# Performance work log

Measured on AMD Instinct MI355X. Metric: run time of the kernel, lower is better.

## Reference

```python
import jax, jax.numpy as jnp
import numpy as np

N_ENTS = 50000
N_EDGES = 500000
N_RELS = 200
RANK = 128
N_LAYERS = 2
RRELU_SLOPE = (1.0 / 8.0 + 1.0 / 3.0) / 2.0  # F.rrelu eval-mode: mean of default lower/upper


def setup_inputs() -> dict:
    key = jax.random.key(0)
    ks = jax.random.split(key, 9)
    return {
        "ent_emb": jax.random.normal(ks[0], (N_ENTS, RANK), dtype=jnp.float32),
        "rel_emb": jax.random.normal(ks[1], (N_RELS, RANK), dtype=jnp.float32),
        "norm": jax.random.uniform(ks[2], (N_ENTS, 1), dtype=jnp.float32),
        "Wn": jax.random.normal(ks[3], (N_LAYERS, RANK, RANK), dtype=jnp.float32) * 0.05,
        "Wl": jax.random.normal(ks[4], (N_LAYERS, RANK, RANK), dtype=jnp.float32) * 0.05,
        "Wa": jax.random.normal(ks[5], (N_LAYERS, RANK, RANK), dtype=jnp.float32) * 0.05,
        "src": jax.random.randint(ks[6], (N_EDGES,), 0, N_ENTS, dtype=jnp.int32),
        "dst": jax.random.randint(ks[7], (N_EDGES,), 0, N_ENTS, dtype=jnp.int32),
        "etype": jax.random.randint(ks[8], (N_EDGES,), 0, N_RELS, dtype=jnp.int32),
    }


def reference(ent_emb, rel_emb, norm, Wn, Wl, Wa, src, dst, etype):
    n = ent_emb.shape[0]
    # in-degree mask (same graph across layers)
    in_deg = jax.ops.segment_sum(jnp.ones_like(dst, dtype=jnp.float32), dst, num_segments=n)
    has_in = (in_deg > 0)[:, None]  # [N,1]
    h = ent_emb
    for l in range(Wn.shape[0]):
        # edge gather + add + linear: msg = (h[src] + rel_emb[etype]) @ Wn[l]
        msg = (h[src] + rel_emb[etype]) @ Wn[l]  # [E, rank]
        # scatter-sum into destination nodes, then per-node norm
        agg = jax.ops.segment_sum(msg, dst, num_segments=n) * norm  # [N, rank]
        # masked self-loop: loop_weight where in_degree>0, else alone_loop_weight
        loop = jnp.where(has_in, h @ Wl[l], h @ Wa[l])
        h = agg + loop
        # rrelu in eval mode == leaky relu with slope (1/8 + 1/3)/2
        h = jnp.where(h >= 0, h, h * RRELU_SLOPE)
        # dropout=0.0 -> identity
    return h
```

## Files before the change

### kernel.cpp

```cpp
#include <hip/hip_runtime.h>

#define SLOPE 0.22916666666666666f
#define ALONE_CAP 2048

typedef __attribute__((ext_vector_type(8))) short bfrag;
typedef __attribute__((ext_vector_type(4))) float ffrag;

__device__ __forceinline__ unsigned short rne16(float f) {
    unsigned u = __float_as_uint(f);
    return (unsigned short)((u + 0x7FFFu + ((u >> 16) & 1u)) >> 16);
}
__device__ __forceinline__ float bf2f(unsigned short h) {
    return __uint_as_float(((unsigned)h) << 16);
}
__device__ __forceinline__ unsigned packsplit(float f) {
    unsigned short hi = rne16(f);
    unsigned short lo = rne16(f - bf2f(hi));
    return ((unsigned)hi << 16) | lo;
}
__device__ __forceinline__ float recon(unsigned u) {
    return __uint_as_float(u & 0xFFFF0000u) + __uint_as_float(u << 16);
}
__device__ __forceinline__ float4 recon4(uint4 u) {
    return make_float4(recon(u.x), recon(u.y), recon(u.z), recon(u.w));
}

__global__ __launch_bounds__(256) void prep_kernel(
    const int* __restrict__ dst, int* __restrict__ deg, int e, int eb,
    const float* __restrict__ ent, unsigned* __restrict__ Esp,
    int total4, int cb,
    const float* __restrict__ Wn, const float* __restrict__ Wl,
    ushort* __restrict__ packW) {
    int b = blockIdx.x;
    if (b < eb) {
        int i = b * 256 + threadIdx.x;
        if (i < e) atomicAdd(&deg[dst[i]], 1);
    } else if (b < eb + cb) {
        int i = (b - eb) * 256 + threadIdx.x;
        if (i >= total4) return;
        float4 v = ((const float4*)ent)[i];
        uint4 w;
        w.x = packsplit(v.x); w.y = packsplit(v.y);
        w.z = packsplit(v.z); w.w = packsplit(v.w);
        ((uint4*)Esp)[i] = w;
    } else {
        int t = (b - eb - cb) * 256 + threadIdx.x;
        if (t >= 4 * 4 * 128 * 4) return;
        int quad = t & 3;
        int nn   = (t >> 2) & 127;
        int kc   = (t >> 9) & 3;
        int mat  = t >> 11;
        const float* W = ((mat & 1) ? Wl : Wn) + (mat >> 1) * 16384;
        ushort* oh = packW + mat * 32768;
        ushort* ol = oh + 16384;
        int obase = ((kc * 128 + nn) * 4 + quad) * 8;
        #pragma unroll
        for (int j = 0; j < 8; ++j) {
            float w = W[(kc * 32 + quad * 8 + j) * 128 + nn];
            unsigned short hi = rne16(w);
            oh[obase + j] = hi;
            ol[obase + j] = rne16(w - bf2f(hi));
        }
    }
}

__global__ __launch_bounds__(256) void scan_partial_kernel(const int* __restrict__ deg,
                                                           int* __restrict__ partial, int n) {
    __shared__ int wsum[4];
    int base = blockIdx.x * 1024;
    int t = threadIdx.x;
    int s = 0;
    #pragma unroll
    for (int j = 0; j < 4; ++j) {
        int i = base + t + 256 * j;
        if (i < n) s += deg[i];
    }
    #pragma unroll
    for (int off = 1; off < 64; off <<= 1) s += __shfl_xor(s, off, 64);
    if ((t & 63) == 0) wsum[t >> 6] = s;
    __syncthreads();
    if (t == 0) partial[blockIdx.x] = wsum[0] + wsum[1] + wsum[2] + wsum[3];
}

__global__ __launch_bounds__(256) void scan_final_kernel(const int* __restrict__ deg,
                                                         const int* __restrict__ partial,
                                                         int* __restrict__ row_off,
                                                         int* __restrict__ alone_list,
                                                         int* __restrict__ alone_count, int n) {
    __shared__ int wsum[4];
    __shared__ int sbase;
    int bid = blockIdx.x;
    int t = threadIdx.x, lane = t & 63, wid = t >> 6;
    if (wid == 0) {
        int v = (lane < bid) ? partial[lane] : 0;
        #pragma unroll
        for (int off = 1; off < 64; off <<= 1) v += __shfl_xor(v, off, 64);
        if (lane == 0) sbase = v;
    }
    int base = bid * 1024;
    int i0 = base + t * 4;
    int v0 = (i0 + 0 < n) ? deg[i0 + 0] : 0;
    int v1 = (i0 + 1 < n) ? deg[i0 + 1] : 0;
    int v2 = (i0 + 2 < n) ? deg[i0 + 2] : 0;
    int v3 = (i0 + 3 < n) ? deg[i0 + 3] : 0;
    int s = v0 + v1 + v2 + v3;
    int x = s;
    #pragma unroll
    for (int off = 1; off < 64; off <<= 1) {
        int y = __shfl_up(x, off, 64);
        if (lane >= off) x += y;
    }
    if (lane == 63) wsum[wid] = x;
    __syncthreads();
    int wbase = 0;
    #pragma unroll
    for (int w = 0; w < 4; ++w) { int ws = wsum[w]; if (w < wid) wbase += ws; }
    int p = sbase + wbase + x - s;
    if (i0 + 0 <= n) row_off[i0 + 0] = p;
    p += v0;
    if (i0 + 1 <= n) row_off[i0 + 1] = p;
    p += v1;
    if (i0 + 2 <= n) row_off[i0 + 2] = p;
    p += v2;
    if (i0 + 3 <= n) row_off[i0 + 3] = p;
    if (i0 + 0 < n && v0 == 0) { int q = atomicAdd(alone_count, 1); if (q < ALONE_CAP) alone_list[q] = i0; }
    if (i0 + 1 < n && v1 == 0) { int q = atomicAdd(alone_count, 1); if (q < ALONE_CAP) alone_list[q] = i0 + 1; }
    if (i0 + 2 < n && v2 == 0) { int q = atomicAdd(alone_count, 1); if (q < ALONE_CAP) alone_list[q] = i0 + 2; }
    if (i0 + 3 < n && v3 == 0) { int q = atomicAdd(alone_count, 1); if (q < ALONE_CAP) alone_list[q] = i0 + 3; }
}

__global__ __launch_bounds__(256) void scatter_kernel(
    const int* __restrict__ src, const int* __restrict__ dst,
    const int* __restrict__ ety, const int* __restrict__ row_off,
    int* __restrict__ cursor, unsigned* __restrict__ edges, int e) {
    int i = blockIdx.x * 256 + threadIdx.x;
    if (i < e) {
        int v = dst[i];
        int pos = row_off[v] + atomicAdd(&cursor[v], 1);
        edges[pos] = (unsigned)src[i] | ((unsigned)ety[i] << 16);
    }
}

template <int SPLIT>
__global__ __launch_bounds__(256) void agg_kernel(
    const float* __restrict__ hf, const unsigned* __restrict__ hs,
    const float* __restrict__ rel,
    const float* __restrict__ norm, const int* __restrict__ row_off,
    const unsigned* __restrict__ edges, unsigned* __restrict__ Ssp, int n) {
    int wave = threadIdx.x >> 6, lane = threadIdx.x & 63;
    int v = blockIdx.x * 4 + wave;
    if (v >= n) return;
    int s0 = row_off[v], s1 = row_off[v + 1];
    float nm = norm[v];
    int half = lane >> 5;
    int c4 = (lane & 31) * 4;
    float4 acc = make_float4(0.f, 0.f, 0.f, 0.f);
    int e = s0;
    for (; e + 7 < s1; e += 8) {
        unsigned q0 = edges[e + half];
        unsigned q1 = edges[e + 2 + half];
        unsigned q2 = edges[e + 4 + half];
        unsigned q3 = edges[e + 6 + half];
        float4 h0, h1, h2, h3;
        if (SPLIT) {
            h0 = recon4(*(const uint4*)&hs[(size_t)(q0 & 0xFFFFu) * 128 + c4]);
            h1 = recon4(*(const uint4*)&hs[(size_t)(q1 & 0xFFFFu) * 128 + c4]);
            h2 = recon4(*(const uint4*)&hs[(size_t)(q2 & 0xFFFFu) * 128 + c4]);
            h3 = recon4(*(const uint4*)&hs[(size_t)(q3 & 0xFFFFu) * 128 + c4]);
        } else {
            h0 = *(const float4*)&hf[(size_t)(q0 & 0xFFFFu) * 128 + c4];
            h1 = *(const float4*)&hf[(size_t)(q1 & 0xFFFFu) * 128 + c4];
            h2 = *(const float4*)&hf[(size_t)(q2 & 0xFFFFu) * 128 + c4];
            h3 = *(const float4*)&hf[(size_t)(q3 & 0xFFFFu) * 128 + c4];
        }
        float4 r0 = *(const float4*)&rel[(size_t)(q0 >> 16) * 128 + c4];
        float4 r1 = *(const float4*)&rel[(size_t)(q1 >> 16) * 128 + c4];
        float4 r2 = *(const float4*)&rel[(size_t)(q2 >> 16) * 128 + c4];
        float4 r3 = *(const float4*)&rel[(size_t)(q3 >> 16) * 128 + c4];
        acc.x += ((h0.x + r0.x) + (h1.x + r1.x)) + ((h2.x + r2.x) + (h3.x + r3.x));
        acc.y += ((h0.y + r0.y) + (h1.y + r1.y)) + ((h2.y + r2.y) + (h3.y + r3.y));
        acc.z += ((h0.z + r0.z) + (h1.z + r1.z)) + ((h2.z + r2.z) + (h3.z + r3.z));
        acc.w += ((h0.w + r0.w) + (h1.w + r1.w)) + ((h2.w + r2.w) + (h3.w + r3.w));
    }
    for (; e + 1 < s1; e += 2) {
        unsigned q0 = edges[e + half];
        float4 h0 = SPLIT ? recon4(*(const uint4*)&hs[(size_t)(q0 & 0xFFFFu) * 128 + c4])
                          : *(const float4*)&hf[(size_t)(q0 & 0xFFFFu) * 128 + c4];
        float4 r0 = *(const float4*)&rel[(size_t)(q0 >> 16) * 128 + c4];
        acc.x += h0.x + r0.x; acc.y += h0.y + r0.y;
        acc.z += h0.z + r0.z; acc.w += h0.w + r0.w;
    }
    if (e < s1 && half == 0) {
        unsigned q0 = edges[e];
        float4 h0 = SPLIT ? recon4(*(const uint4*)&hs[(size_t)(q0 & 0xFFFFu) * 128 + c4])
                          : *(const float4*)&hf[(size_t)(q0 & 0xFFFFu) * 128 + c4];
        float4 r0 = *(const float4*)&rel[(size_t)(q0 >> 16) * 128 + c4];
        acc.x += h0.x + r0.x; acc.y += h0.y + r0.y;
        acc.z += h0.z + r0.z; acc.w += h0.w + r0.w;
    }
    acc.x += __shfl_xor(acc.x, 32, 64);
    acc.y += __shfl_xor(acc.y, 32, 64);
    acc.z += __shfl_xor(acc.z, 32, 64);
    acc.w += __shfl_xor(acc.w, 32, 64);
    if (half == 0) {
        uint4 w;
        w.x = packsplit(acc.x * nm); w.y = packsplit(acc.y * nm);
        w.z = packsplit(acc.z * nm); w.w = packsplit(acc.w * nm);
        *(uint4*)&Ssp[(size_t)v * 128 + c4] = w;
    }
}

__global__ __launch_bounds__(256, 3) void gemm_mfma_kernel(
    const unsigned* __restrict__ Ssp, const unsigned* Hsp,
    const ushort* __restrict__ Pnh, const ushort* __restrict__ Pnl,
    const ushort* __restrict__ Plh, const ushort* __restrict__ Pll,
    float* __restrict__ out, unsigned* Osp, int n) {
    const int tid = threadIdx.x;
    const int wave = tid >> 6, lane = tid & 63;
    const int quad = lane >> 4, l16 = lane & 15;
    const int row_base = blockIdx.x * 64 + wave * 16;

    int r0c = row_base + l16;
    if (r0c > n - 1) r0c = n - 1;
    const size_t arow = (size_t)r0c * 128;

    ffrag acc[8];
    #pragma unroll
    for (int ct = 0; ct < 8; ++ct) acc[ct] = (ffrag)0.f;

    uint4 a_cur0 = *(const uint4*)(Ssp + arow + quad * 8);
    uint4 a_cur1 = *(const uint4*)(Ssp + arow + quad * 8 + 4);

    #pragma unroll 1
    for (int it = 0; it < 8; ++it) {
        const int kc = it & 3;
        const ushort* Pbh = (it >= 4) ? Plh : Pnh;
        const ushort* Pbl = (it >= 4) ? Pll : Pnl;

        uint4 a_nxt0, a_nxt1;
        if (it < 7) {
            const unsigned* An = (it + 1 >= 4) ? Hsp : Ssp;
            const int koffn = ((it + 1) & 3) * 32 + quad * 8;
            a_nxt0 = *(const uint4*)(An + arow + koffn);
            a_nxt1 = *(const uint4*)(An + arow + koffn + 4);
        }

        bfrag bh[8], bl[8];
        #pragma unroll
        for (int ct = 0; ct < 8; ++ct) {
            int bidx = ((kc * 128 + ct * 16 + l16) * 4 + quad) * 8;
            bh[ct] = *(const bfrag*)(Pbh + bidx);
            bl[ct] = *(const bfrag*)(Pbl + bidx);
        }

        bfrag ah, al;
        #pragma unroll
        for (int j = 0; j < 4; ++j) {
            unsigned u0 = ((const unsigned*)&a_cur0)[j];
            unsigned u1 = ((const unsigned*)&a_cur1)[j];
            ah[j]     = (short)(u0 >> 16); al[j]     = (short)(u0 & 0xFFFFu);
            ah[j + 4] = (short)(u1 >> 16); al[j + 4] = (short)(u1 & 0xFFFFu);
        }

        #pragma unroll
        for (int ct = 0; ct < 8; ++ct)
            acc[ct] = __builtin_amdgcn_mfma_f32_16x16x32_bf16(ah, bh[ct], acc[ct], 0, 0, 0);
        #pragma unroll
        for (int ct = 0; ct < 8; ++ct)
            acc[ct] = __builtin_amdgcn_mfma_f32_16x16x32_bf16(ah, bl[ct], acc[ct], 0, 0, 0);
        #pragma unroll
        for (int ct = 0; ct < 8; ++ct)
            acc[ct] = __builtin_amdgcn_mfma_f32_16x16x32_bf16(al, bh[ct], acc[ct], 0, 0, 0);

        a_cur0 = a_nxt0;
        a_cur1 = a_nxt1;
    }

    #pragma unroll
    for (int ct = 0; ct < 8; ++ct) {
        #pragma unroll
        for (int rg = 0; rg < 4; ++rg) {
            int r = row_base + quad * 4 + rg;
            if (r < n) {
                int c = ct * 16 + l16;
                float v = acc[ct][rg];
                v = v >= 0.f ? v : v * SLOPE;
                if (out) out[(size_t)r * 128 + c] = v;
                if (Osp) Osp[(size_t)r * 128 + c] = packsplit(v);
            }
        }
    }
}

__global__ __launch_bounds__(128) void fixup_kernel(
    const float* __restrict__ Hrows, int by_node,
    const float* __restrict__ Wa,
    const int* __restrict__ alone_list, const int* __restrict__ alone_count,
    float* out, unsigned* Osp, float* asave) {
    int cnt = *alone_count;
    if (cnt > ALONE_CAP) cnt = ALONE_CAP;
    int t = threadIdx.x;
    for (int i = blockIdx.x; i < cnt; i += gridDim.x) {
        int v = alone_list[i];
        const float* hrow = Hrows + (size_t)(by_node ? v : i) * 128;
        float acc = 0.f;
        for (int k = 0; k < 128; ++k)
            acc += hrow[k] * Wa[k * 128 + t];
        float o = acc >= 0.f ? acc : acc * SLOPE;
        if (out) out[(size_t)v * 128 + t] = o;
        if (Osp) Osp[(size_t)v * 128 + t] = packsplit(o);
        if (asave) asave[(size_t)i * 128 + t] = o;
    }
}

extern "C" void kernel_launch(void* const* d_in, const int* in_sizes, int n_in,
                              void* d_out, int out_size, void* d_ws, size_t ws_size,
                              hipStream_t stream) {
    const float* ent  = (const float*)d_in[0];
    const float* rel  = (const float*)d_in[1];
    const float* norm = (const float*)d_in[2];
    const float* Wn   = (const float*)d_in[3];
    const float* Wl   = (const float*)d_in[4];
    const float* Wa   = (const float*)d_in[5];
    const int*   src  = (const int*)d_in[6];
    const int*   dst  = (const int*)d_in[7];
    const int*   ety  = (const int*)d_in[8];
    float* out = (float*)d_out;

    const int n = in_sizes[2];
    const int e = in_sizes[7];

    char* ws = (char*)d_ws;
    int* deg         = (int*)ws;
    int* cursor      = deg + n;
    int* alone_count = cursor + n;
    size_t zbytes = (size_t)(2 * n + 1) * sizeof(int);
    size_t p = (zbytes + 255) & ~(size_t)255;
    int* row_off = (int*)(ws + p);
    p += (((size_t)(n + 1) * 4) + 255) & ~(size_t)255;
    int* partial = (int*)(ws + p);
    p += 256;
    int* alone_list = (int*)(ws + p);
    p += (((size_t)ALONE_CAP * 4) + 255) & ~(size_t)255;
    float* asave = (float*)(ws + p);
    p += (((size_t)ALONE_CAP * 128 * 4) + 255) & ~(size_t)255;
    unsigned* edges = (unsigned*)(ws + p);
    p += (((size_t)e * 4) + 255) & ~(size_t)255;
    unsigned* Ssp = (unsigned*)(ws + p);
    p += (((size_t)n * 128 * 4) + 255) & ~(size_t)255;
    unsigned* Esp = (unsigned*)(ws + p);
    p += (((size_t)n * 128 * 4) + 255) & ~(size_t)255;
    ushort* packW = (ushort*)(ws + p);
    p += 4 * 32768 * 2;

    const int eb = (e + 255) / 256;
    const int cb = (n * 32 + 255) / 256;
    const int nparts = (n + 1023) / 1024;
    const int gb = (n + 63) / 64;
    const int ab = (n + 3) / 4;

    hipMemsetAsync(ws, 0, zbytes, stream);
    prep_kernel<<<eb + cb + 32, 256, 0, stream>>>(dst, deg, e, eb,
                                                  ent, Esp, n * 32, cb,
                                                  Wn, Wl, packW);
    scan_partial_kernel<<<nparts, 256, 0, stream>>>(deg, partial, n);
    scan_final_kernel<<<nparts, 256, 0, stream>>>(deg, partial, row_off,
                                                  alone_list, alone_count, n);
    scatter_kernel<<<eb, 256, 0, stream>>>(src, dst, ety, row_off, cursor, edges, e);

    agg_kernel<0><<<ab, 256, 0, stream>>>(ent, nullptr, rel, norm, row_off, edges, Ssp, n);
    gemm_mfma_kernel<<<gb, 256, 0, stream>>>(Ssp, Esp,
                                             packW, packW + 16384,
                                             packW + 32768, packW + 49152,
                                             nullptr, Esp, n);
    fixup_kernel<<<16, 128, 0, stream>>>(ent, 1, Wa, alone_list, alone_count,
                                         nullptr, Esp, asave);

    agg_kernel<1><<<ab, 256, 0, stream>>>(nullptr, Esp, rel, norm, row_off, edges, Ssp, n);
    gemm_mfma_kernel<<<gb, 256, 0, stream>>>(Ssp, Esp,
                                             packW + 65536, packW + 81920,
                                             packW + 98304, packW + 114688,
                                             out, nullptr, n);
    fixup_kernel<<<16, 128, 0, stream>>>(asave, 0, Wa + 16384, alone_list, alone_count,
                                         out, nullptr, nullptr);
}
```

Before: 316.5 us.

## Process three 16-row tiles per wave in MFMA GEMM to reuse B fragments

Each wave now computes 48 output rows (three 16-row tiles) instead of 16, so every B-fragment load from the packed weights feeds three times as many MFMAs. Block tile grows to 192 rows and the grid shrinks to match, while launch bounds drop occupancy to 2 blocks to make room for the larger accumulator set (24 ffrags). This cuts redundant weight loads per row, at the cost of higher register pressure, lower occupancy and fewer blocks.

```diff
diff --git a/kernel.cpp b/kernel.cpp
--- a/kernel.cpp
+++ b/kernel.cpp
@@ -210,7 +210,7 @@
     }
 }
 
-__global__ __launch_bounds__(256, 3) void gemm_mfma_kernel(
+__global__ __launch_bounds__(256, 2) void gemm_mfma_kernel(
     const unsigned* __restrict__ Ssp, const unsigned* Hsp,
     const ushort* __restrict__ Pnh, const ushort* __restrict__ Pnl,
     const ushort* __restrict__ Plh, const ushort* __restrict__ Pll,
@@ -218,18 +218,28 @@
     const int tid = threadIdx.x;
     const int wave = tid >> 6, lane = tid & 63;
     const int quad = lane >> 4, l16 = lane & 15;
-    const int row_base = blockIdx.x * 64 + wave * 16;
-
-    int r0c = row_base + l16;
-    if (r0c > n - 1) r0c = n - 1;
-    const size_t arow = (size_t)r0c * 128;
-
-    ffrag acc[8];
-    #pragma unroll
-    for (int ct = 0; ct < 8; ++ct) acc[ct] = (ffrag)0.f;
-
-    uint4 a_cur0 = *(const uint4*)(Ssp + arow + quad * 8);
-    uint4 a_cur1 = *(const uint4*)(Ssp + arow + quad * 8 + 4);
+    const int row_base = blockIdx.x * 192 + wave * 48;
+
+    size_t arow[3];
+    #pragma unroll
+    for (int rt = 0; rt < 3; ++rt) {
+        int r = row_base + rt * 16 + l16;
+        if (r > n - 1) r = n - 1;
+        arow[rt] = (size_t)r * 128;
+    }
+
+    ffrag acc[3][8];
+    #pragma unroll
+    for (int rt = 0; rt < 3; ++rt)
+        #pragma unroll
+        for (int ct = 0; ct < 8; ++ct) acc[rt][ct] = (ffrag)0.f;
+
+    uint4 a0[3], a1[3];
+    #pragma unroll
+    for (int rt = 0; rt < 3; ++rt) {
+        a0[rt] = *(const uint4*)(Ssp + arow[rt] + quad * 8);
+        a1[rt] = *(const uint4*)(Ssp + arow[rt] + quad * 8 + 4);
+    }
 
     #pragma unroll 1
     for (int it = 0; it < 8; ++it) {
@@ -237,12 +247,15 @@
         const ushort* Pbh = (it >= 4) ? Plh : Pnh;
         const ushort* Pbl = (it >= 4) ? Pll : Pnl;
 
-        uint4 a_nxt0, a_nxt1;
+        uint4 na0[3], na1[3];
         if (it < 7) {
             const unsigned* An = (it + 1 >= 4) ? Hsp : Ssp;
             const int koffn = ((it + 1) & 3) * 32 + quad * 8;
-            a_nxt0 = *(const uint4*)(An + arow + koffn);
-            a_nxt1 = *(const uint4*)(An + arow + koffn + 4);
+            #pragma unroll
+            for (int rt = 0; rt < 3; ++rt) {
+                na0[rt] = *(const uint4*)(An + arow[rt] + koffn);
+                na1[rt] = *(const uint4*)(An + arow[rt] + koffn + 4);
+            }
         }
 
         bfrag bh[8], bl[8];
@@ -253,40 +266,52 @@
             bl[ct] = *(const bfrag*)(Pbl + bidx);
         }
 
-        bfrag ah, al;
-        #pragma unroll
-        for (int j = 0; j < 4; ++j) {
-            unsigned u0 = ((const unsigned*)&a_cur0)[j];
-            unsigned u1 = ((const unsigned*)&a_cur1)[j];
-            ah[j]     = (short)(u0 >> 16); al[j]     = (short)(u0 & 0xFFFFu);
-            ah[j + 4] = (short)(u1 >> 16); al[j + 4] = (short)(u1 & 0xFFFFu);
-        }
-
-        #pragma unroll
-        for (int ct = 0; ct < 8; ++ct)
-            acc[ct] = __builtin_amdgcn_mfma_f32_16x16x32_bf16(ah, bh[ct], acc[ct], 0, 0, 0);
-        #pragma unroll
-        for (int ct = 0; ct < 8; ++ct)
-            acc[ct] = __builtin_amdgcn_mfma_f32_16x16x32_bf16(ah, bl[ct], acc[ct], 0, 0, 0);
-        #pragma unroll
-        for (int ct = 0; ct < 8; ++ct)
-            acc[ct] = __builtin_amdgcn_mfma_f32_16x16x32_bf16(al, bh[ct], acc[ct], 0, 0, 0);
-
-        a_cur0 = a_nxt0;
-        a_cur1 = a_nxt1;
-    }
-
-    #pragma unroll
-    for (int ct = 0; ct < 8; ++ct) {
-        #pragma unroll
-        for (int rg = 0; rg < 4; ++rg) {
-            int r = row_base + quad * 4 + rg;
-            if (r < n) {
-                int c = ct * 16 + l16;
-                float v = acc[ct][rg];
-                v = v >= 0.f ? v : v * SLOPE;
-                if (out) out[(size_t)r * 128 + c] = v;
-                if (Osp) Osp[(size_t)r * 128 + c] = packsplit(v);
+        bfrag ah[3], al[3];
+        #pragma unroll
+        for (int rt = 0; rt < 3; ++rt) {
+            #pragma unroll
+            for (int j = 0; j < 4; ++j) {
+                unsigned u0 = ((const unsigned*)&a0[rt])[j];
+                unsigned u1 = ((const unsigned*)&a1[rt])[j];
+                ah[rt][j]     = (short)(u0 >> 16); al[rt][j]     = (short)(u0 & 0xFFFFu);
+                ah[rt][j + 4] = (short)(u1 >> 16); al[rt][j + 4] = (short)(u1 & 0xFFFFu);
+            }
+        }
+
+        #pragma unroll
+        for (int rt = 0; rt < 3; ++rt)
+            #pragma unroll
+            for (int ct = 0; ct < 8; ++ct)
+                acc[rt][ct] = __builtin_amdgcn_mfma_f32_16x16x32_bf16(ah[rt], bh[ct], acc[rt][ct], 0, 0, 0);
+        #pragma unroll
+        for (int rt = 0; rt < 3; ++rt)
+            #pragma unroll
+            for (int ct = 0; ct < 8; ++ct)
+                acc[rt][ct] = __builtin_amdgcn_mfma_f32_16x16x32_bf16(ah[rt], bl[ct], acc[rt][ct], 0, 0, 0);
+        #pragma unroll
+        for (int rt = 0; rt < 3; ++rt)
+            #pragma unroll
+            for (int ct = 0; ct < 8; ++ct)
+                acc[rt][ct] = __builtin_amdgcn_mfma_f32_16x16x32_bf16(al[rt], bh[ct], acc[rt][ct], 0, 0, 0);
+
+        #pragma unroll
+        for (int rt = 0; rt < 3; ++rt) { a0[rt] = na0[rt]; a1[rt] = na1[rt]; }
+    }
+
+    #pragma unroll
+    for (int rt = 0; rt < 3; ++rt) {
+        #pragma unroll
+        for (int ct = 0; ct < 8; ++ct) {
+            #pragma unroll
+            for (int rg = 0; rg < 4; ++rg) {
+                int r = row_base + rt * 16 + quad * 4 + rg;
+                if (r < n) {
+                    int c = ct * 16 + l16;
+                    float v = acc[rt][ct][rg];
+                    v = v >= 0.f ? v : v * SLOPE;
+                    if (out) out[(size_t)r * 128 + c] = v;
+                    if (Osp) Osp[(size_t)r * 128 + c] = packsplit(v);
+                }
             }
         }
     }
@@ -356,7 +381,7 @@
     const int eb = (e + 255) / 256;
     const int cb = (n * 32 + 255) / 256;
     const int nparts = (n + 1023) / 1024;
-    const int gb = (n + 63) / 64;
+    const int gb = (n + 191) / 192;
     const int ab = (n + 3) / 4;
 
     hipMemsetAsync(ws, 0, zbytes, stream);
```

Result: faster. 306.2 us (-3.2%).

## Stage packed weight fragments in double-buffered LDS for MFMA GEMM

Applied to the files above, without the earlier changes.

Reorders the packed bf16 hi/lo weight layout so that each MFMA column-tile fragment is contiguous per lane. The GEMM kernel now cooperatively loads each K-chunk of weights into double-buffered shared memory, prefetching the next chunk into registers while the current one is used. Previously each wave read B fragments straight from global memory. The aim is to share weight loads across the four waves and cut global/L2 traffic, at the cost of 32KB of LDS per block (which may limit occupancy under launch_bounds 3) and a barrier on every iteration.

```diff
diff --git a/kernel.cpp b/kernel.cpp
--- a/kernel.cpp
+++ b/kernel.cpp
@@ -53,7 +53,7 @@
         const float* W = ((mat & 1) ? Wl : Wn) + (mat >> 1) * 16384;
         ushort* oh = packW + mat * 32768;
         ushort* ol = oh + 16384;
-        int obase = ((kc * 128 + nn) * 4 + quad) * 8;
+        int obase = kc * 4096 + (nn >> 4) * 512 + (quad * 16 + (nn & 15)) * 8;
         #pragma unroll
         for (int j = 0; j < 8; ++j) {
             float w = W[(kc * 32 + quad * 8 + j) * 128 + nn];
@@ -215,6 +215,8 @@
     const ushort* __restrict__ Pnh, const ushort* __restrict__ Pnl,
     const ushort* __restrict__ Plh, const ushort* __restrict__ Pll,
     float* __restrict__ out, unsigned* Osp, int n) {
+    __shared__ ushort ldsB[2][2][4096];
+
     const int tid = threadIdx.x;
     const int wave = tid >> 6, lane = tid & 63;
     const int quad = lane >> 4, l16 = lane & 15;
@@ -228,17 +230,39 @@
     #pragma unroll
     for (int ct = 0; ct < 8; ++ct) acc[ct] = (ffrag)0.f;
 
+    {
+        uint4 t0 = *(const uint4*)(Pnh + tid * 8);
+        uint4 t1 = *(const uint4*)(Pnh + 2048 + tid * 8);
+        uint4 t2 = *(const uint4*)(Pnl + tid * 8);
+        uint4 t3 = *(const uint4*)(Pnl + 2048 + tid * 8);
+        *(uint4*)&ldsB[0][0][tid * 8] = t0;
+        *(uint4*)&ldsB[0][0][2048 + tid * 8] = t1;
+        *(uint4*)&ldsB[0][1][tid * 8] = t2;
+        *(uint4*)&ldsB[0][1][2048 + tid * 8] = t3;
+    }
+
     uint4 a_cur0 = *(const uint4*)(Ssp + arow + quad * 8);
     uint4 a_cur1 = *(const uint4*)(Ssp + arow + quad * 8 + 4);
 
+    __syncthreads();
+
+    int cur = 0;
     #pragma unroll 1
     for (int it = 0; it < 8; ++it) {
-        const int kc = it & 3;
-        const ushort* Pbh = (it >= 4) ? Plh : Pnh;
-        const ushort* Pbl = (it >= 4) ? Pll : Pnl;
+        uint4 s0, s1, s2, s3;
+        const bool have = (it < 7);
+        if (have) {
+            const int itn = it + 1;
+            const ushort* nh = ((itn >= 4) ? Plh : Pnh) + (itn & 3) * 4096;
+            const ushort* nl = ((itn >= 4) ? Pll : Pnl) + (itn & 3) * 4096;
+            s0 = *(const uint4*)(nh + tid * 8);
+            s1 = *(const uint4*)(nh + 2048 + tid * 8);
+            s2 = *(const uint4*)(nl + tid * 8);
+            s3 = *(const uint4*)(nl + 2048 + tid * 8);
+        }
 
         uint4 a_nxt0, a_nxt1;
-        if (it < 7) {
+        if (have) {
             const unsigned* An = (it + 1 >= 4) ? Hsp : Ssp;
             const int koffn = ((it + 1) & 3) * 32 + quad * 8;
             a_nxt0 = *(const uint4*)(An + arow + koffn);
@@ -248,9 +272,8 @@
         bfrag bh[8], bl[8];
         #pragma unroll
         for (int ct = 0; ct < 8; ++ct) {
-            int bidx = ((kc * 128 + ct * 16 + l16) * 4 + quad) * 8;
-            bh[ct] = *(const bfrag*)(Pbh + bidx);
-            bl[ct] = *(const bfrag*)(Pbl + bidx);
+            bh[ct] = *(const bfrag*)&ldsB[cur][0][ct * 512 + lane * 8];
+            bl[ct] = *(const bfrag*)&ldsB[cur][1][ct * 512 + lane * 8];
         }
 
         bfrag ah, al;
@@ -272,8 +295,17 @@
         for (int ct = 0; ct < 8; ++ct)
             acc[ct] = __builtin_amdgcn_mfma_f32_16x16x32_bf16(al, bh[ct], acc[ct], 0, 0, 0);
 
+        if (have) {
+            *(uint4*)&ldsB[cur ^ 1][0][tid * 8] = s0;
+            *(uint4*)&ldsB[cur ^ 1][0][2048 + tid * 8] = s1;
+            *(uint4*)&ldsB[cur ^ 1][1][tid * 8] = s2;
+            *(uint4*)&ldsB[cur ^ 1][1][2048 + tid * 8] = s3;
+        }
+        __syncthreads();
+
         a_cur0 = a_nxt0;
         a_cur1 = a_nxt1;
+        cur ^= 1;
     }
 
     #pragma unroll
```

Result: faster. 278.1 us (-12.1%).

## Stage packed weight fragments in double-buffered LDS for MFMA GEMM

Applied to the files above, without the earlier changes.

The packed B-weight layout is reordered so each 16-column tile forms a contiguous 512-element block. The GEMM kernel then loads two k-chunks of hi/lo weights cooperatively into double-buffered shared memory, prefetching the next stage while computing the current one. Previously each wave read B fragments directly from global memory. This shares weight loads across the block's four waves and overlaps loads with MFMA work, but uses 64KB of LDS and adds barriers, so occupancy drops to 2 blocks per CU.

```diff
diff --git a/kernel.cpp b/kernel.cpp
--- a/kernel.cpp
+++ b/kernel.cpp
@@ -53,7 +53,7 @@
         const float* W = ((mat & 1) ? Wl : Wn) + (mat >> 1) * 16384;
         ushort* oh = packW + mat * 32768;
         ushort* ol = oh + 16384;
-        int obase = ((kc * 128 + nn) * 4 + quad) * 8;
+        int obase = kc * 4096 + (nn >> 4) * 512 + (quad * 16 + (nn & 15)) * 8;
         #pragma unroll
         for (int j = 0; j < 8; ++j) {
             float w = W[(kc * 32 + quad * 8 + j) * 128 + nn];
@@ -210,11 +210,13 @@
     }
 }
 
-__global__ __launch_bounds__(256, 3) void gemm_mfma_kernel(
+__global__ __launch_bounds__(256, 2) void gemm_mfma_kernel(
     const unsigned* __restrict__ Ssp, const unsigned* Hsp,
     const ushort* __restrict__ Pnh, const ushort* __restrict__ Pnl,
     const ushort* __restrict__ Plh, const ushort* __restrict__ Pll,
     float* __restrict__ out, unsigned* Osp, int n) {
+    __shared__ ushort ldsB[2][2][2][4096];
+
     const int tid = threadIdx.x;
     const int wave = tid >> 6, lane = tid & 63;
     const int quad = lane >> 4, l16 = lane & 15;
@@ -228,52 +230,101 @@
     #pragma unroll
     for (int ct = 0; ct < 8; ++ct) acc[ct] = (ffrag)0.f;
 
-    uint4 a_cur0 = *(const uint4*)(Ssp + arow + quad * 8);
-    uint4 a_cur1 = *(const uint4*)(Ssp + arow + quad * 8 + 4);
+    uint4 acur[2][2];
+
+    {
+        uint4 s00, s01, s10, s11, s20, s21, s30, s31;
+        acur[0][0] = *(const uint4*)(Ssp + arow + 0 * 32 + quad * 8);
+        acur[0][1] = *(const uint4*)(Ssp + arow + 0 * 32 + quad * 8 + 4);
+        acur[1][0] = *(const uint4*)(Ssp + arow + 1 * 32 + quad * 8);
+        acur[1][1] = *(const uint4*)(Ssp + arow + 1 * 32 + quad * 8 + 4);
+        s00 = *(const uint4*)(Pnh + 0 * 4096 + tid * 8);
+        s01 = *(const uint4*)(Pnh + 0 * 4096 + 2048 + tid * 8);
+        s10 = *(const uint4*)(Pnl + 0 * 4096 + tid * 8);
+        s11 = *(const uint4*)(Pnl + 0 * 4096 + 2048 + tid * 8);
+        s20 = *(const uint4*)(Pnh + 1 * 4096 + tid * 8);
+        s21 = *(const uint4*)(Pnh + 1 * 4096 + 2048 + tid * 8);
+        s30 = *(const uint4*)(Pnl + 1 * 4096 + tid * 8);
+        s31 = *(const uint4*)(Pnl + 1 * 4096 + 2048 + tid * 8);
+        *(uint4*)&ldsB[0][0][0][tid * 8] = s00;
+        *(uint4*)&ldsB[0][0][0][2048 + tid * 8] = s01;
+        *(uint4*)&ldsB[0][0][1][tid * 8] = s10;
+        *(uint4*)&ldsB[0][0][1][2048 + tid * 8] = s11;
+        *(uint4*)&ldsB[0][1][0][tid * 8] = s20;
+        *(uint4*)&ldsB[0][1][0][2048 + tid * 8] = s21;
+        *(uint4*)&ldsB[0][1][1][tid * 8] = s30;
+        *(uint4*)&ldsB[0][1][1][2048 + tid * 8] = s31;
+    }
+    __syncthreads();
 
     #pragma unroll 1
-    for (int it = 0; it < 8; ++it) {
-        const int kc = it & 3;
-        const ushort* Pbh = (it >= 4) ? Plh : Pnh;
-        const ushort* Pbl = (it >= 4) ? Pll : Pnl;
-
-        uint4 a_nxt0, a_nxt1;
-        if (it < 7) {
-            const unsigned* An = (it + 1 >= 4) ? Hsp : Ssp;
-            const int koffn = ((it + 1) & 3) * 32 + quad * 8;
-            a_nxt0 = *(const uint4*)(An + arow + koffn);
-            a_nxt1 = *(const uint4*)(An + arow + koffn + 4);
-        }
-
-        bfrag bh[8], bl[8];
+    for (int ms = 0; ms < 4; ++ms) {
+        const int buf = ms & 1;
+
+        uint4 snxt[2][2][2];
+        uint4 anxt[2][2];
+        const bool have = (ms < 3);
+        if (have) {
+            const int msn = ms + 1;
+            const ushort* Pbh = (msn >= 2) ? Plh : Pnh;
+            const ushort* Pbl = (msn >= 2) ? Pll : Pnl;
+            const unsigned* An = (msn >= 2) ? Hsp : Ssp;
+            #pragma unroll
+            for (int kk = 0; kk < 2; ++kk) {
+                const int kc = (msn & 1) * 2 + kk;
+                anxt[kk][0] = *(const uint4*)(An + arow + kc * 32 + quad * 8);
+                anxt[kk][1] = *(const uint4*)(An + arow + kc * 32 + quad * 8 + 4);
+                snxt[kk][0][0] = *(const uint4*)(Pbh + kc * 4096 + tid * 8);
+                snxt[kk][0][1] = *(const uint4*)(Pbh + kc * 4096 + 2048 + tid * 8);
+                snxt[kk][1][0] = *(const uint4*)(Pbl + kc * 4096 + tid * 8);
+                snxt[kk][1][1] = *(const uint4*)(Pbl + kc * 4096 + 2048 + tid * 8);
+            }
+        }
+
         #pragma unroll
-        for (int ct = 0; ct < 8; ++ct) {
-            int bidx = ((kc * 128 + ct * 16 + l16) * 4 + quad) * 8;
-            bh[ct] = *(const bfrag*)(Pbh + bidx);
-            bl[ct] = *(const bfrag*)(Pbl + bidx);
-        }
-
-        bfrag ah, al;
-        #pragma unroll
-        for (int j = 0; j < 4; ++j) {
-            unsigned u0 = ((const unsigned*)&a_cur0)[j];
-            unsigned u1 = ((const unsigned*)&a_cur1)[j];
-            ah[j]     = (short)(u0 >> 16); al[j]     = (short)(u0 & 0xFFFFu);
-            ah[j + 4] = (short)(u1 >> 16); al[j + 4] = (short)(u1 & 0xFFFFu);
-        }
-
-        #pragma unroll
-        for (int ct = 0; ct < 8; ++ct)
-            acc[ct] = __builtin_amdgcn_mfma_f32_16x16x32_bf16(ah, bh[ct], acc[ct], 0, 0, 0);
-        #pragma unroll
-        for (int ct = 0; ct < 8; ++ct)
-            acc[ct] = __builtin_amdgcn_mfma_f32_16x16x32_bf16(ah, bl[ct], acc[ct], 0, 0, 0);
-        #pragma unroll
-        for (int ct = 0; ct < 8; ++ct)
-            acc[ct] = __builtin_amdgcn_mfma_f32_16x16x32_bf16(al, bh[ct], acc[ct], 0, 0, 0);
-
-        a_cur0 = a_nxt0;
-        a_cur1 = a_nxt1;
+        for (int kk = 0; kk < 2; ++kk) {
+            bfrag bh[8], bl[8];
+            #pragma unroll
+            for (int ct = 0; ct < 8; ++ct) {
+                bh[ct] = *(const bfrag*)&ldsB[buf][kk][0][ct * 512 + lane * 8];
+                bl[ct] = *(const bfrag*)&ldsB[buf][kk][1][ct * 512 + lane * 8];
+            }
+            bfrag ah, al;
+            #pragma unroll
+            for (int j = 0; j < 4; ++j) {
+                unsigned u0 = ((const unsigned*)&acur[kk][0])[j];
+                unsigned u1 = ((const unsigned*)&acur[kk][1])[j];
+                ah[j]     = (short)(u0 >> 16); al[j]     = (short)(u0 & 0xFFFFu);
+                ah[j + 4] = (short)(u1 >> 16); al[j + 4] = (short)(u1 & 0xFFFFu);
+            }
+            #pragma unroll
+            for (int ct = 0; ct < 8; ++ct)
+                acc[ct] = __builtin_amdgcn_mfma_f32_16x16x32_bf16(ah, bh[ct], acc[ct], 0, 0, 0);
+            #pragma unroll
+            for (int ct = 0; ct < 8; ++ct)
+                acc[ct] = __builtin_amdgcn_mfma_f32_16x16x32_bf16(ah, bl[ct], acc[ct], 0, 0, 0);
+            #pragma unroll
+            for (int ct = 0; ct < 8; ++ct)
+                acc[ct] = __builtin_amdgcn_mfma_f32_16x16x32_bf16(al, bh[ct], acc[ct], 0, 0, 0);
+        }
+
+        if (have) {
+            #pragma unroll
+            for (int kk = 0; kk < 2; ++kk) {
+                *(uint4*)&ldsB[buf ^ 1][kk][0][tid * 8] = snxt[kk][0][0];
+                *(uint4*)&ldsB[buf ^ 1][kk][0][2048 + tid * 8] = snxt[kk][0][1];
+                *(uint4*)&ldsB[buf ^ 1][kk][1][tid * 8] = snxt[kk][1][0];
+                *(uint4*)&ldsB[buf ^ 1][kk][1][2048 + tid * 8] = snxt[kk][1][1];
+            }
+        }
+        __syncthreads();
+        if (have) {
+            #pragma unroll
+            for (int kk = 0; kk < 2; ++kk) {
+                acur[kk][0] = anxt[kk][0];
+                acur[kk][1] = anxt[kk][1];
+            }
+        }
     }
 
     #pragma unroll
```

Result: slower. 324.1 us (+2.4%).
